# Optimization experiments

Hardware: AMD Instinct MI355X
Metric: run time of the kernel (lower is better)

Reference implementation:

```python
import jax, jax.numpy as jnp
import numpy as np

B, N, DF, E, H = 8, 2048, 128, 128, 4  # batch, nodes, feat, dim_gnn, n_gnn heads


def setup_inputs() -> dict:
    key = jax.random.key(0)
    ks = jax.random.split(key, 11)
    s = 0.05
    return {
        "x": jax.random.normal(ks[0], (B, N, DF), jnp.float32),
        "emb1_W": jax.random.normal(ks[1], (E, N), jnp.float32) * s,
        "emb1_b": jax.random.normal(ks[2], (E,), jnp.float32) * s,
        "wq_W": jax.random.normal(ks[3], (H, E, E), jnp.float32) * s,
        "wq_b": jax.random.normal(ks[4], (H, E), jnp.float32) * s,
        "wk_W": jax.random.normal(ks[5], (H, E, E), jnp.float32) * s,
        "wk_b": jax.random.normal(ks[6], (H, E), jnp.float32) * s,
        "wv_W": jax.random.normal(ks[7], (H, E, E), jnp.float32) * s,
        "wv_b": jax.random.normal(ks[8], (H, E), jnp.float32) * s,
        "emb2_W": jax.random.normal(ks[9], (E, H * E), jnp.float32) * s,
        "emb2_b": jax.random.normal(ks[10], (E,), jnp.float32) * s,
    }


def reference(x, emb1_W, emb1_b, wq_W, wq_b, wk_W, wk_b, wv_W, wv_b, emb2_W, emb2_b):
    # pairwise node-info matrix: [B, N, N]
    info = jnp.einsum('bnd,bmd->bnm', x, x)
    # first arbitrary embedding: Linear(N -> E)
    emb = jnp.einsum('bnm,em->bne', info, emb1_W) + emb1_b  # [B, N, E]
    # all heads at once (Linear: y = x W^T + b)
    q = jnp.einsum('bne,hfe->bhnf', emb, wq_W) + wq_b[None, :, None, :]
    # k is computed in the original but never used (bug preserved)
    k = jnp.einsum('bne,hfe->bhnf', emb, wk_W) + wk_b[None, :, None, :]
    v = jnp.einsum('bne,hfe->bhnf', emb, wv_W) + wv_b[None, :, None, :]
    scale = jnp.sqrt(jnp.asarray(E, q.dtype))
    # original passes (q, v, info): attn = tanh((q @ v^T @ info) / sqrt(E))
    qv = jnp.einsum('bhnf,bhmf->bhnm', q, v)          # [B, H, N, N]
    attn = jnp.tanh(jnp.einsum('bhnm,bmp->bhnp', qv, info) / scale)
    h = jnp.einsum('bhnp,bhpf->bhnf', attn, v)        # [B, H, N, E]
    # concat heads on last dim (head-major ordering matches torch.cat)
    hcat = h.transpose(0, 2, 1, 3).reshape(B, N, H * E)
    out = jnp.einsum('bnf,ef->bne', hcat, emb2_W) + emb2_b
    return jax.nn.relu(out)
```

## Files before the change

kernel.cpp:

```cpp
#include <hip/hip_runtime.h>
#include <math.h>


typedef float f32x4 __attribute__((ext_vector_type(4)));

static constexpr int BB = 8, NN = 2048, DD = 128, EE = 128, HH = 4;

struct ZMap { int div; int mod; long long str; };

enum { E_STORE = 0, E_BCOL = 1, E_BROW = 2, E_TANH = 3, E_RELU = 4, E_ATOM = 5 };

__global__ void transp_x(const float* __restrict__ x, float* __restrict__ xT) {
  __shared__ float t[32][33];
  const int b = blockIdx.z, n0 = blockIdx.y * 32, d0 = blockIdx.x * 32;
  const int tr = threadIdx.x >> 3, tc = (threadIdx.x & 7) * 4;
  f32x4 v = *(const f32x4*)(x + ((long long)b * NN + n0 + tr) * DD + d0 + tc);
  t[tr][tc + 0] = v[0]; t[tr][tc + 1] = v[1];
  t[tr][tc + 2] = v[2]; t[tr][tc + 3] = v[3];
  __syncthreads();
  f32x4 o = { t[tc + 0][tr], t[tc + 1][tr], t[tc + 2][tr], t[tc + 3][tr] };
  *(f32x4*)(xT + ((long long)b * DD + d0 + tr) * NN + n0 + tc) = o;
}

template <int EPI>
__launch_bounds__(256)
__global__ void gemm32(const float* __restrict__ A, ZMap za,
                       const float* __restrict__ Bt, ZMap zb,
                       float* __restrict__ C, ZMap zc, ZMap zc2,
                       const float* __restrict__ bias, ZMap ze,
                       int K, int ksplit, int lda, int ldb, int ldc, float scale) {
  constexpr int LD = 132;
  __shared__ float As[16 * LD];
  __shared__ float Bs[16 * LD];
  const int tid = threadIdx.x;
  const int z = blockIdx.z;
  const int kc = z % ksplit, kn = K / ksplit, k0 = kc * kn;
  const float* Ab = A + (long long)((z / za.div) % za.mod) * za.str +
                    (long long)blockIdx.y * 128 * lda;
  const float* Bb = Bt + (long long)((z / zb.div) % zb.mod) * zb.str +
                    (long long)blockIdx.x * 128 * ldb;
  const int ty = tid >> 4, tx = tid & 15;

  float acc[8][8] = {};
  for (int kk = k0; kk < k0 + kn; kk += 16) {
#pragma unroll
    for (int i = 0; i < 2; ++i) {
      int g = i * 256 + tid, r = g >> 2, c = (g & 3) * 4;
      f32x4 va = *(const f32x4*)(Ab + (long long)r * lda + kk + c);
      f32x4 vb = *(const f32x4*)(Bb + (long long)r * ldb + kk + c);
#pragma unroll
      for (int j = 0; j < 4; ++j) {
        As[(c + j) * LD + r] = va[j];
        Bs[(c + j) * LD + r] = vb[j];
      }
    }
    __syncthreads();
#pragma unroll
    for (int k = 0; k < 16; ++k) {
      f32x4 a0 = *(const f32x4*)(As + k * LD + ty * 8);
      f32x4 a1 = *(const f32x4*)(As + k * LD + ty * 8 + 4);
      f32x4 b0 = *(const f32x4*)(Bs + k * LD + tx * 8);
      f32x4 b1 = *(const f32x4*)(Bs + k * LD + tx * 8 + 4);
      float ar[8] = { a0[0], a0[1], a0[2], a0[3], a1[0], a1[1], a1[2], a1[3] };
      float br[8] = { b0[0], b0[1], b0[2], b0[3], b1[0], b1[1], b1[2], b1[3] };
#pragma unroll
      for (int i = 0; i < 8; ++i)
#pragma unroll
        for (int j = 0; j < 8; ++j)
          acc[i][j] += ar[i] * br[j];
    }
    __syncthreads();
  }

  long long coff = (long long)((z / zc.div) % zc.mod) * zc.str +
                   (long long)((z / zc2.div) % zc2.mod) * zc2.str;
  const float* bp = bias ? bias + (long long)((z / ze.div) % ze.mod) * ze.str : nullptr;
#pragma unroll
  for (int i = 0; i < 8; ++i) {
    int row = (int)blockIdx.y * 128 + ty * 8 + i;
#pragma unroll
    for (int j = 0; j < 8; ++j) {
      int col = (int)blockIdx.x * 128 + tx * 8 + j;
      float v = acc[i][j];
      long long off = coff + (long long)row * ldc + col;
      if constexpr (EPI == E_ATOM) {
        atomicAdd(C + off, v);
      } else if constexpr (EPI == E_TANH) {
        float a = fminf(fmaxf(v * scale, -15.f), 15.f);
        float e = __expf(2.f * a);
        C[off] = (e - 1.f) / (e + 1.f);
      } else {
        if constexpr (EPI == E_BCOL) v += bp[col];
        if constexpr (EPI == E_BROW) v += bp[row];
        if constexpr (EPI == E_RELU) v = fmaxf(v + bp[col], 0.f);
        C[off] = v;
      }
    }
  }
}

extern "C" void kernel_launch(void* const* d_in, const int* in_sizes, int n_in,
                              void* d_out, int out_size, void* d_ws, size_t ws_size,
                              hipStream_t stream) {
  const float* x   = (const float*)d_in[0];
  const float* e1W = (const float*)d_in[1];
  const float* e1b = (const float*)d_in[2];
  const float* wqW = (const float*)d_in[3];
  const float* wqb = (const float*)d_in[4];
  const float* wvW = (const float*)d_in[7];
  const float* wvb = (const float*)d_in[8];
  const float* e2W = (const float*)d_in[9];
  const float* e2b = (const float*)d_in[10];

  const size_t MB = 1 << 20;
  const long long S_x = (long long)NN * DD;
  const long long S_e = (long long)NN * EE;
  const long long S_info = (long long)NN * NN;
  const long long S_hc = (long long)NN * HH * EE;
  const long long S_w = (long long)EE * DD;
  const float rs = 0.08838834764831845f;
  const ZMap Z0{1, 1, 0};

  struct Cfg { int bch, g; };
  const Cfg cfgs[] = {{8,4},{8,2},{8,1},{4,2},{4,1},{2,1},{1,1}};
  int BCH = 1, G = 1;
  for (const Cfg& c : cfgs) {
    size_t per_b = (size_t)(S_w * 5 + S_x + S_e * 13 + S_hc) * 4;
    size_t need = (size_t)c.bch * per_b + (size_t)c.g * S_info * 4 + 2 * MB;
    if (need <= ws_size) { BCH = c.bch; G = c.g; break; }
  }
  const int NBH = 4 * BCH;

  char* p = (char*)d_ws;
  auto carve = [&](size_t bytes) {
    char* r = p; p += (bytes + 255) & ~(size_t)255; return r;
  };
  float* G1T  = (float*)carve((size_t)BCH * S_w * 4);
  float* T2T  = (float*)carve((size_t)NBH * S_w * 4);
  float* hcat = (float*)carve((size_t)BCH * S_hc * 4);
  size_t zero_span = (size_t)(p - (char*)G1T);
  float* xT   = (float*)carve((size_t)BCH * S_x * 4);
  float* emb  = (float*)carve((size_t)BCH * S_e * 4);
  float* q    = (float*)carve((size_t)NBH * S_e * 4);
  float* vT   = (float*)carve((size_t)NBH * S_e * 4);
  float* WT   = (float*)carve((size_t)NBH * S_e * 4);
  float* attn = (float*)carve((size_t)G * S_info * 4);

  for (int bc = 0; bc < BB / BCH; ++bc) {
    const float* xc = x + (long long)bc * BCH * S_x;
    hipMemsetAsync(G1T, 0, zero_span, stream);
    transp_x<<<dim3(DD / 32, NN / 32, BCH), dim3(256), 0, stream>>>(xc, xT);

    gemm32<E_ATOM><<<dim3(1, 1, BCH * 16), 256, 0, stream>>>(
        e1W, Z0, xT, ZMap{16, BCH, S_x}, G1T, ZMap{16, BCH, S_w}, Z0,
        nullptr, Z0, 2048, 16, 2048, 2048, 128, 0.f);
    gemm32<E_BCOL><<<dim3(1, 16, BCH), 256, 0, stream>>>(
        xc, ZMap{1, BCH, S_x}, G1T, ZMap{1, BCH, S_w}, emb, ZMap{1, BCH, S_e}, Z0,
        e1b, Z0, 128, 1, 128, 128, 128, 0.f);
    gemm32<E_BCOL><<<dim3(1, 16, NBH), 256, 0, stream>>>(
        emb, ZMap{4, BCH, S_e}, wqW, ZMap{1, 4, S_w}, q, ZMap{1, NBH, S_e}, Z0,
        wqb, ZMap{1, 4, EE}, 128, 1, 128, 128, 128, 0.f);
    gemm32<E_BROW><<<dim3(16, 1, NBH), 256, 0, stream>>>(
        wvW, ZMap{1, 4, S_w}, emb, ZMap{4, BCH, S_e}, vT, ZMap{1, NBH, S_e}, Z0,
        wvb, ZMap{1, 4, EE}, 128, 1, 128, 128, 2048, 0.f);
    gemm32<E_ATOM><<<dim3(1, 1, NBH * 16), 256, 0, stream>>>(
        vT, ZMap{16, NBH, S_e}, xT, ZMap{64, BCH, S_x}, T2T, ZMap{16, NBH, S_w}, Z0,
        nullptr, Z0, 2048, 16, 2048, 2048, 128, 0.f);
    gemm32<E_STORE><<<dim3(1, 16, NBH), 256, 0, stream>>>(
        xc, ZMap{4, BCH, S_x}, T2T, ZMap{1, NBH, S_w}, WT, ZMap{1, NBH, S_e}, Z0,
        nullptr, Z0, 128, 1, 128, 128, 128, 0.f);
    for (int c = 0; c < NBH / G; ++c) {
      long long o = (long long)c * G;
      gemm32<E_TANH><<<dim3(16, 16, G), 256, 0, stream>>>(
          q + o * S_e, ZMap{1, 32, S_e}, WT + o * S_e, ZMap{1, 32, S_e},
          attn, ZMap{1, 32, S_info}, Z0, nullptr, Z0,
          128, 1, 128, 128, 2048, rs);
      gemm32<E_ATOM><<<dim3(1, 16, G * 4), 256, 0, stream>>>(
          attn, ZMap{4, 32, S_info}, vT + o * S_e, ZMap{4, 32, S_e},
          hcat + (o >> 2) * S_hc + (o & 3) * 128, ZMap{16, BCH, S_hc},
          ZMap{4, 4, 128}, nullptr, Z0, 2048, 4, 2048, 2048, 512, 0.f);
    }
    gemm32<E_RELU><<<dim3(1, 16, BCH), 256, 0, stream>>>(
        hcat, ZMap{1, BCH, S_hc}, e2W, Z0,
        (float*)d_out + (long long)bc * BCH * S_e, ZMap{1, BCH, S_e}, Z0,
        e2b, Z0, 512, 1, 512, 512, 128, 0.f);
  }
}
```

Before: 2.559 ms.

## Use split-bf16 MFMA for the q·W^T tanh attention GEMM

Replaces the FP32 SIMT GEMM that produces the tanh attention matrix with a kernel using bf16 MFMA 16x16x32 instructions. Each fp32 operand is split into high and low bf16 parts, and three MFMA products (hi*hi, hi*lo, lo*hi) are summed to get close to fp32 accuracy. Operands are loaded straight from global memory into registers without LDS staging, which may mean redundant global loads across waves. This GEMM has K=128, so the tanh attention write of 2048x2048 per head may dominate its cost anyway, and the larger atomic GEMM that follows is unchanged.

Result: slower. 2.650 ms (+3.6%).

```diff
diff --git a/kernel.cpp b/kernel.cpp
--- a/kernel.cpp
+++ b/kernel.cpp
@@ -3,6 +3,7 @@
 
 
 typedef float f32x4 __attribute__((ext_vector_type(4)));
+typedef short short8 __attribute__((ext_vector_type(8)));
 
 static constexpr int BB = 8, NN = 2048, DD = 128, EE = 128, HH = 4;
 
@@ -97,6 +98,86 @@
       }
     }
   }
+}
+
+__device__ __forceinline__ unsigned short f2bf(float v) {
+  unsigned u = __float_as_uint(v);
+  unsigned r = u + 0x7FFFu + ((u >> 16) & 1u);
+  return (unsigned short)(r >> 16);
+}
+__device__ __forceinline__ float bf2f(unsigned short b) {
+  return __uint_as_float(((unsigned)b) << 16);
+}
+
+__launch_bounds__(256)
+__global__ void gemm_spb_tanh(const float* __restrict__ A, ZMap za,
+                              const float* __restrict__ Bt, ZMap zb,
+                              float* __restrict__ C, ZMap zc,
+                              int K, int lda, int ldb, int ldc, float scale) {
+  const int tid = threadIdx.x;
+  const int z = blockIdx.z;
+  const int lane = tid & 63;
+  const int wr = tid >> 7, wcq = (tid >> 6) & 1;
+  const int lr = lane & 15, lg = lane >> 4;
+  const float* Ab = A + (long long)((z / za.div) % za.mod) * za.str +
+                    (long long)(blockIdx.y * 128 + wr * 64 + lr) * lda;
+  const float* Bb = Bt + (long long)((z / zb.div) % zb.mod) * zb.str +
+                    (long long)(blockIdx.x * 128 + wcq * 64 + lr) * ldb;
+
+  f32x4 accH[4][4] = {};
+  f32x4 accL[4][4] = {};
+  for (int kk = 0; kk < K; kk += 32) {
+    short8 ah[4], al[4], bh[4], bl[4];
+#pragma unroll
+    for (int m = 0; m < 4; ++m) {
+      const float* pa = Ab + (long long)m * 16 * lda + kk + lg * 8;
+      f32x4 v0 = *(const f32x4*)pa, v1 = *(const f32x4*)(pa + 4);
+#pragma unroll
+      for (int j = 0; j < 8; ++j) {
+        float v = (j < 4) ? v0[j] : v1[j - 4];
+        unsigned short hb = f2bf(v);
+        float hif = bf2f(hb);
+        ah[m][j] = (short)hb;
+        al[m][j] = (short)f2bf(v - hif);
+      }
+    }
+#pragma unroll
+    for (int n = 0; n < 4; ++n) {
+      const float* pb = Bb + (long long)n * 16 * ldb + kk + lg * 8;
+      f32x4 v0 = *(const f32x4*)pb, v1 = *(const f32x4*)(pb + 4);
+#pragma unroll
+      for (int j = 0; j < 8; ++j) {
+        float v = (j < 4) ? v0[j] : v1[j - 4];
+        unsigned short hb = f2bf(v);
+        float hif = bf2f(hb);
+        bh[n][j] = (short)hb;
+        bl[n][j] = (short)f2bf(v - hif);
+      }
+    }
+#pragma unroll
+    for (int m = 0; m < 4; ++m)
+#pragma unroll
+      for (int n = 0; n < 4; ++n) {
+        accH[m][n] = __builtin_amdgcn_mfma_f32_16x16x32_bf16(ah[m], bh[n], accH[m][n], 0, 0, 0);
+        accL[m][n] = __builtin_amdgcn_mfma_f32_16x16x32_bf16(ah[m], bl[n], accL[m][n], 0, 0, 0);
+        accL[m][n] = __builtin_amdgcn_mfma_f32_16x16x32_bf16(al[m], bh[n], accL[m][n], 0, 0, 0);
+      }
+  }
+
+  long long coff = (long long)((z / zc.div) % zc.mod) * zc.str;
+#pragma unroll
+  for (int m = 0; m < 4; ++m)
+#pragma unroll
+    for (int n = 0; n < 4; ++n)
+#pragma unroll
+      for (int j = 0; j < 4; ++j) {
+        int row = (int)blockIdx.y * 128 + wr * 64 + m * 16 + lg * 4 + j;
+        int col = (int)blockIdx.x * 128 + wcq * 64 + n * 16 + lr;
+        float v = accH[m][n][j] + accL[m][n][j];
+        float a = fminf(fmaxf(v * scale, -15.f), 15.f);
+        float e = __expf(2.f * a);
+        C[coff + (long long)row * ldc + col] = (e - 1.f) / (e + 1.f);
+      }
 }
 
 extern "C" void kernel_launch(void* const* d_in, const int* in_sizes, int n_in,
@@ -171,10 +252,9 @@
         nullptr, Z0, 128, 1, 128, 128, 128, 0.f);
     for (int c = 0; c < NBH / G; ++c) {
       long long o = (long long)c * G;
-      gemm32<E_TANH><<<dim3(16, 16, G), 256, 0, stream>>>(
+      gemm_spb_tanh<<<dim3(16, 16, G), 256, 0, stream>>>(
           q + o * S_e, ZMap{1, 32, S_e}, WT + o * S_e, ZMap{1, 32, S_e},
-          attn, ZMap{1, 32, S_info}, Z0, nullptr, Z0,
-          128, 1, 128, 128, 2048, rs);
+          attn, ZMap{1, 32, S_info}, 128, 128, 128, 2048, rs);
       gemm32<E_ATOM><<<dim3(1, 16, G * 4), 256, 0, stream>>>(
           attn, ZMap{4, 32, S_info}, vT + o * S_e, ZMap{4, 32, S_e},
           hcat + (o >> 2) * S_hc + (o & 3) * 128, ZMap{16, BCH, S_hc},
```
